# Performance work log

Hardware: AMD Instinct MI355X
Metric: run time of the kernel (lower is better)

The kernel has to match this reference:

```python
import jax, jax.numpy as jnp
import numpy as np

B, K, DIM = 20000, 32, 256
N_ENT, N_USR = 100000, 50000

def _norm_clip(e):
    # torch nn.Embedding(max_norm=1): renormalize looked-up rows to norm <= 1
    n = jnp.linalg.norm(e, axis=-1, keepdims=True)
    return e * jnp.minimum(1.0, 1.0 / jnp.maximum(n, 1e-12))

def setup_inputs() -> dict:
    key = jax.random.key(0)
    ks = jax.random.split(key, 7)
    return {
        "u": jax.random.randint(ks[0], (B,), 0, N_USR),
        "t_idx": jax.random.randint(ks[1], (B,), 0, N_ENT),
        "n_idx": jax.random.randint(ks[2], (B, K), 0, N_ENT),
        "entity_emb": jax.random.normal(ks[3], (N_ENT, DIM), jnp.float32) * 0.1,
        "user_emb": jax.random.normal(ks[4], (N_USR, DIM), jnp.float32) * 0.1,
        "W": jax.random.normal(ks[5], (DIM // 2, DIM), jnp.float32) * 0.05,
        "a": jax.random.normal(ks[6], (DIM,), jnp.float32) * 0.05,
    }

def reference(u, t_idx, n_idx, entity_emb, user_emb, W, a):
    d_half = W.shape[0]
    xt = _norm_clip(entity_emb[t_idx])          # [B, D]
    xn = _norm_clip(entity_emb[n_idx])          # [B, K, D]
    tw = xt @ W.T                               # [B, H]  H = D/2
    nw = jnp.einsum('bkd,hd->bkh', xn, W)       # [B, K, H]
    # a(cat([tw, nw])) = tw @ a[:H] + nw @ a[H:]
    scores = tw @ a[:d_half]                    # [B]
    scores = scores[:, None] + nw @ a[d_half:]  # [B, K]
    e = jnp.where(scores >= 0, scores, 0.2 * scores)  # leaky relu, slope 0.2
    alpha = jax.nn.softmax(e, axis=1)           # softmax over neighbors
    head = jnp.einsum('bk,bkh->bh', alpha, nw)  # [B, H]
    # both "heads" share W and a in the original -> identical outputs, concat
    items = jnp.concatenate([head, head], axis=-1)  # [B, D]
    users = _norm_clip(user_emb[u])             # [B, D]
    uv = jnp.sum(users * items, axis=1)
    return jax.nn.sigmoid(uv)
```

## Files before the change

kernel.cpp:

```cpp
#include <hip/hip_runtime.h>
#include <math.h>

#define B_    20000
#define K_    32
#define DIM_  256
#define H_    128
#define NENT_ 100000

typedef unsigned int   uint_t;
typedef unsigned short ushort_t;
typedef __attribute__((ext_vector_type(8))) short bf16x8;
typedef __attribute__((ext_vector_type(4))) float f32x4;

__device__ __forceinline__ float dot4(float4 a, float4 b) {
    return a.x * b.x + a.y * b.y + a.z * b.z + a.w * b.w;
}

__device__ __forceinline__ float wred64(float v) {
    #pragma unroll
    for (int m = 32; m >= 1; m >>= 1) v += __shfl_xor(v, m, 64);
    return v;
}

__device__ __forceinline__ ushort_t f2bf(float f) {
    uint_t x = __float_as_uint(f);
    uint_t r = (x + 0x7fffu + ((x >> 16) & 1u)) >> 16;
    return (ushort_t)r;
}

__device__ __forceinline__ uint_t pack2(float lo, float hi) {
    return (uint_t)f2bf(lo) | ((uint_t)f2bf(hi) << 16);
}

__launch_bounds__(256)
__global__ void proj_direct(const float* __restrict__ ent,
                            const float* __restrict__ Wm,
                            const float* __restrict__ av,
                            float* __restrict__ sc1,
                            float* __restrict__ sc2,
                            ushort_t* __restrict__ P) {
    __shared__ short Ws[128 * 256];

    const int t    = threadIdx.x;
    const int gb   = blockIdx.x * 128;
    const int lane = t & 63;
    const int w    = t >> 6;
    const int l15  = lane & 15;
    const int l4   = lane >> 4;

    {
        const int r    = t >> 1;
        const int half = (t & 1) * 128;
        const float* wp = Wm + r * DIM_ + half;
        const int swz = (r & 7) << 4;
        #pragma unroll
        for (int jc = 0; jc < 16; ++jc) {
            float4 f0 = *(const float4*)(wp + jc * 8);
            float4 f1 = *(const float4*)(wp + jc * 8 + 4);
            union { bf16x8 v; ushort_t us[8]; } pk;
            pk.us[0] = f2bf(f0.x); pk.us[1] = f2bf(f0.y);
            pk.us[2] = f2bf(f0.z); pk.us[3] = f2bf(f0.w);
            pk.us[4] = f2bf(f1.x); pk.us[5] = f2bf(f1.y);
            pk.us[6] = f2bf(f1.z); pk.us[7] = f2bf(f1.w);
            const int off = (r * 512 + half * 2 + jc * 16) ^ swz;
            *(bf16x8*)((char*)Ws + off) = pk.v;
        }
    }

    const int ebase = gb + w * 32;
    bf16x8 bfr[2][8];
    float scale[2];
    #pragma unroll
    for (int et = 0; et < 2; ++et) {
        const int eg = min(ebase + et * 16 + l15, NENT_ - 1);
        const float* xp = ent + (size_t)eg * DIM_ + l4 * 8;
        float ssq = 0.f;
        #pragma unroll
        for (int kk = 0; kk < 8; ++kk) {
            float4 f0 = *(const float4*)(xp + kk * 32);
            float4 f1 = *(const float4*)(xp + kk * 32 + 4);
            ssq += dot4(f0, f0) + dot4(f1, f1);
            union { bf16x8 v; ushort_t us[8]; } pk;
            pk.us[0] = f2bf(f0.x); pk.us[1] = f2bf(f0.y);
            pk.us[2] = f2bf(f0.z); pk.us[3] = f2bf(f0.w);
            pk.us[4] = f2bf(f1.x); pk.us[5] = f2bf(f1.y);
            pk.us[6] = f2bf(f1.z); pk.us[7] = f2bf(f1.w);
            bfr[et][kk] = pk.v;
        }
        ssq += __shfl_xor(ssq, 16, 64);
        ssq += __shfl_xor(ssq, 32, 64);
        scale[et] = fminf(1.f, 1.f / fmaxf(sqrtf(ssq), 1e-12f));
    }

    __syncthreads();

    float s1[2] = {0.f, 0.f}, s2[2] = {0.f, 0.f};
    #pragma unroll 2
    for (int ht = 0; ht < 8; ++ht) {
        const int hrow = ht * 16 + l15;
        const int hswz = (hrow & 7) << 4;
        bf16x8 af[8];
        #pragma unroll
        for (int kk = 0; kk < 8; ++kk)
            af[kk] = *(const bf16x8*)((const char*)Ws +
                     ((hrow * 512 + kk * 64 + l4 * 16) ^ hswz));
        f32x4 acc0 = (f32x4){0.f, 0.f, 0.f, 0.f};
        f32x4 acc1 = (f32x4){0.f, 0.f, 0.f, 0.f};
        #pragma unroll
        for (int kk = 0; kk < 8; ++kk) {
            acc0 = __builtin_amdgcn_mfma_f32_16x16x32_bf16(af[kk], bfr[0][kk], acc0, 0, 0, 0);
            acc1 = __builtin_amdgcn_mfma_f32_16x16x32_bf16(af[kk], bfr[1][kk], acc1, 0, 0, 0);
        }
        const int hb = ht * 16 + l4 * 4;
        const float4 a1v = *(const float4*)(av + hb);
        const float4 a2v = *(const float4*)(av + H_ + hb);
        #pragma unroll
        for (int et = 0; et < 2; ++et) {
            const f32x4 v = et ? acc1 : acc0;
            const float scl = scale[et];
            const float v0 = v[0] * scl, v1 = v[1] * scl;
            const float v2 = v[2] * scl, v3 = v[3] * scl;
            s1[et] += a1v.x * v0 + a1v.y * v1 + a1v.z * v2 + a1v.w * v3;
            s2[et] += a2v.x * v0 + a2v.y * v1 + a2v.z * v2 + a2v.w * v3;
            const int eg = ebase + et * 16 + l15;
            if (eg < NENT_) {
                uint2 pk;
                pk.x = pack2(v0, v1);
                pk.y = pack2(v2, v3);
                *(uint2*)(P + (size_t)eg * H_ + hb) = pk;
            }
        }
    }

    #pragma unroll
    for (int et = 0; et < 2; ++et) {
        float a1 = s1[et], a2 = s2[et];
        a1 += __shfl_xor(a1, 16, 64);
        a1 += __shfl_xor(a1, 32, 64);
        a2 += __shfl_xor(a2, 16, 64);
        a2 += __shfl_xor(a2, 32, 64);
        const int eg = ebase + et * 16 + l15;
        if (l4 == 0 && eg < NENT_) {
            sc1[eg] = a1;
            sc2[eg] = a2;
        }
    }
}

__launch_bounds__(256)
__global__ void main_kernel(const int* __restrict__ u,
                            const int* __restrict__ t_idx,
                            const int* __restrict__ n_idx,
                            const float* __restrict__ usr,
                            const float* __restrict__ sc1,
                            const float* __restrict__ sc2,
                            const ushort_t* __restrict__ P,
                            float* __restrict__ out) {
    const int wave = threadIdx.x >> 6;
    const int lane = threadIdx.x & 63;
    const int b    = blockIdx.x * 4 + wave;
    const int j    = lane & 31;
    const int q    = lane >> 4;
    const int c    = lane & 15;

    const int nk = n_idx[b * K_ + j];
    int nm[8];
    #pragma unroll
    for (int i = 0; i < 8; ++i) nm[i] = __shfl(nk, i * 4 + q);
    uint4 pv[8];
    #pragma unroll
    for (int i = 0; i < 8; ++i)
        pv[i] = *(const uint4*)((const char*)P + (size_t)nm[i] * 256 + c * 16);

    const float* ubp = usr + (size_t)u[b] * DIM_;
    float4 ua0 = *(const float4*)(ubp + 8 * c);
    float4 ua1 = *(const float4*)(ubp + 8 * c + 4);
    float4 ub0 = *(const float4*)(ubp + H_ + 8 * c);
    float4 ub1 = *(const float4*)(ubp + H_ + 8 * c + 4);

    float s = sc1[t_idx[b]] + sc2[nk];
    s = (s >= 0.f) ? s : 0.2f * s;
    float mx = s;
    #pragma unroll
    for (int m = 16; m >= 1; m >>= 1) mx = fmaxf(mx, __shfl_xor(mx, m, 64));
    float ex = __expf(s - mx);
    float sm = ex;
    #pragma unroll
    for (int m = 16; m >= 1; m >>= 1) sm += __shfl_xor(sm, m, 64);
    const float alpha = ex / sm;

    float ss = dot4(ua0, ua0) + dot4(ua1, ua1) + dot4(ub0, ub0) + dot4(ub1, ub1);
    #pragma unroll
    for (int m = 8; m >= 1; m >>= 1) ss += __shfl_xor(ss, m, 64);
    const float scl = fminf(1.f, 1.f / fmaxf(sqrtf(ss), 1e-12f));
    float uc[8];
    uc[0] = scl * (ua0.x + ub0.x); uc[1] = scl * (ua0.y + ub0.y);
    uc[2] = scl * (ua0.z + ub0.z); uc[3] = scl * (ua0.w + ub0.w);
    uc[4] = scl * (ua1.x + ub1.x); uc[5] = scl * (ua1.y + ub1.y);
    uc[6] = scl * (ua1.z + ub1.z); uc[7] = scl * (ua1.w + ub1.w);

    float sp = 0.f;
    #pragma unroll
    for (int i = 0; i < 8; ++i) {
        const float am = __shfl(alpha, i * 4 + q);
        const uint4 v = pv[i];
        float d;
        d  = uc[0] * __uint_as_float(v.x << 16);
        d += uc[1] * __uint_as_float(v.x & 0xffff0000u);
        d += uc[2] * __uint_as_float(v.y << 16);
        d += uc[3] * __uint_as_float(v.y & 0xffff0000u);
        d += uc[4] * __uint_as_float(v.z << 16);
        d += uc[5] * __uint_as_float(v.z & 0xffff0000u);
        d += uc[6] * __uint_as_float(v.w << 16);
        d += uc[7] * __uint_as_float(v.w & 0xffff0000u);
        sp += am * d;
    }
    sp = wred64(sp);
    if (lane == 0) out[b] = 1.f / (1.f + __expf(-sp));
}

__global__ void precompute_v12(const float* __restrict__ W,
                               const float* __restrict__ a,
                               float* __restrict__ v12) {
    int d = blockIdx.x * blockDim.x + threadIdx.x;
    if (d >= DIM_) return;
    float acc1 = 0.f, acc2 = 0.f;
    for (int h = 0; h < H_; ++h) {
        float w = W[h * DIM_ + d];
        acc1 += a[h] * w;
        acc2 += a[H_ + h] * w;
    }
    v12[d] = acc1;
    v12[DIM_ + d] = acc2;
}

__launch_bounds__(256)
__global__ void gat_main(const int* __restrict__ u,
                         const int* __restrict__ t_idx,
                         const int* __restrict__ n_idx,
                         const float* __restrict__ ent,
                         const float* __restrict__ usr,
                         const float* __restrict__ W,
                         const float* __restrict__ v12,
                         float* __restrict__ out) {
    const int b    = blockIdx.x;
    const int tid  = threadIdx.x;
    const int wave = tid >> 6;
    const int lane = tid & 63;

    __shared__ float xn_s[K_][DIM_];
    __shared__ float scr_s[K_];
    __shared__ float alpha_s[K_];
    __shared__ float uc_s[H_];
    __shared__ float red_s[4];

    const float4 v1_4 = ((const float4*)v12)[lane];
    const float4 v2_4 = ((const float4*)(v12 + DIM_))[lane];

    const int t = t_idx[b];
    float4 t4 = ((const float4*)(ent + (size_t)t * DIM_))[lane];
    float ss_t = wred64(dot4(t4, t4));
    float scl_t = fminf(1.0f, 1.0f / fmaxf(sqrtf(ss_t), 1e-12f));
    float s0 = scl_t * wred64(dot4(t4, v1_4));

    const int uid = u[b];
    float4 u4 = ((const float4*)(usr + (size_t)uid * DIM_))[lane];
    float ss_u = wred64(dot4(u4, u4));
    float scl_u = fminf(1.0f, 1.0f / fmaxf(sqrtf(ss_u), 1e-12f));
    float px = __shfl(u4.x, lane + 32);
    float py = __shfl(u4.y, lane + 32);
    float pz = __shfl(u4.z, lane + 32);
    float pw = __shfl(u4.w, lane + 32);
    if (wave == 0 && lane < 32) {
        float4 uc4;
        uc4.x = scl_u * (u4.x + px);
        uc4.y = scl_u * (u4.y + py);
        uc4.z = scl_u * (u4.z + pz);
        uc4.w = scl_u * (u4.w + pw);
        ((float4*)uc_s)[lane] = uc4;
    }

    for (int kk = 0; kk < 8; ++kk) {
        const int k   = wave * 8 + kk;
        const int idx = n_idx[b * K_ + k];
        float4 e4 = ((const float4*)(ent + (size_t)idx * DIM_))[lane];
        float ssk = wred64(dot4(e4, e4));
        float sk  = fminf(1.0f, 1.0f / fmaxf(sqrtf(ssk), 1e-12f));
        float dv2 = wred64(dot4(e4, v2_4));
        float4 xs;
        xs.x = e4.x * sk; xs.y = e4.y * sk; xs.z = e4.z * sk; xs.w = e4.w * sk;
        ((float4*)xn_s[k])[lane] = xs;
        if (lane == 0) {
            float sc = s0 + sk * dv2;
            scr_s[k] = (sc >= 0.f) ? sc : 0.2f * sc;
        }
    }
    __syncthreads();

    if (tid < 32) {
        float e = scr_s[tid];
        float mx = e;
        #pragma unroll
        for (int m = 16; m >= 1; m >>= 1) mx = fmaxf(mx, __shfl_xor(mx, m, 64));
        float ex = expf(e - mx);
        float sm = ex;
        #pragma unroll
        for (int m = 16; m >= 1; m >>= 1) sm += __shfl_xor(sm, m, 64);
        alpha_s[tid] = ex / sm;
    }
    __syncthreads();

    float m_d = 0.f;
    #pragma unroll
    for (int k = 0; k < K_; ++k) m_d += alpha_s[k] * xn_s[k][tid];

    const float* wcol = W + tid;
    float acc = 0.f;
    #pragma unroll 4
    for (int hh = 0; hh < H_; ++hh) acc += uc_s[hh] * wcol[(size_t)hh * DIM_];

    float p = wred64(acc * m_d);
    if (lane == 0) red_s[wave] = p;
    __syncthreads();
    if (tid == 0) {
        float uv = red_s[0] + red_s[1] + red_s[2] + red_s[3];
        out[b] = 1.0f / (1.0f + expf(-uv));
    }
}

extern "C" void kernel_launch(void* const* d_in, const int* in_sizes, int n_in,
                              void* d_out, int out_size, void* d_ws, size_t ws_size,
                              hipStream_t stream) {
    const int*   u     = (const int*)d_in[0];
    const int*   t_idx = (const int*)d_in[1];
    const int*   n_idx = (const int*)d_in[2];
    const float* ent   = (const float*)d_in[3];
    const float* usr   = (const float*)d_in[4];
    const float* W     = (const float*)d_in[5];
    const float* a     = (const float*)d_in[6];
    float*       out   = (float*)d_out;

    const size_t SC1_OFF = 0;
    const size_t SC2_OFF = (size_t)NENT_ * 4;
    const size_t P_OFF   = (size_t)NENT_ * 8;
    const size_t NEED    = P_OFF + (size_t)NENT_ * H_ * 2;

    if (ws_size >= NEED) {
        float*    sc1 = (float*)((char*)d_ws + SC1_OFF);
        float*    sc2 = (float*)((char*)d_ws + SC2_OFF);
        ushort_t* P   = (ushort_t*)((char*)d_ws + P_OFF);

        hipLaunchKernelGGL(proj_direct, dim3((NENT_ + 127) / 128), dim3(256), 0, stream,
                           ent, W, a, sc1, sc2, P);
        hipLaunchKernelGGL(main_kernel, dim3(B_ / 4), dim3(256), 0, stream,
                           u, t_idx, n_idx, usr, sc1, sc2, P, out);
    } else {
        float* v12 = (float*)d_ws;
        hipLaunchKernelGGL(precompute_v12, dim3(1), dim3(256), 0, stream, W, a, v12);
        hipLaunchKernelGGL(gat_main, dim3(B_), dim3(256), 0, stream,
                           u, t_idx, n_idx, ent, usr, W, v12, out);
    }
}
```

Measured before the change: 237.7 us.

## Pre-convert W to bf16 fragment layout and drop LDS staging in projection

A small prep kernel converts W to bf16 once and stores it in MFMA fragment order in workspace. The projection kernel then reads the A fragments straight from global memory (L2-resident, 64KB) instead of every block converting all of W into a 64KB LDS tile and syncing. Dropping the LDS allocation also allows higher occupancy (launch_bounds 256,4). In exchange it adds an extra launch and repeated global/L2 reads of W per wave, and the workspace requirement grows, which could fall back to the slow path if the workspace is too small.

After: 262.5 us. +10.4%, slower.

```diff
diff --git a/kernel.cpp b/kernel.cpp
--- a/kernel.cpp
+++ b/kernel.cpp
@@ -32,42 +32,38 @@
     return (uint_t)f2bf(lo) | ((uint_t)f2bf(hi) << 16);
 }
 
-__launch_bounds__(256)
-__global__ void proj_direct(const float* __restrict__ ent,
-                            const float* __restrict__ Wm,
-                            const float* __restrict__ av,
-                            float* __restrict__ sc1,
-                            float* __restrict__ sc2,
-                            ushort_t* __restrict__ P) {
-    __shared__ short Ws[128 * 256];
-
+__global__ void w_prep(const float* __restrict__ Wm, ushort_t* __restrict__ Wb) {
+    const int idx  = blockIdx.x * 256 + threadIdx.x;
+    const int lane = idx & 63;
+    const int kk   = (idx >> 6) & 7;
+    const int ht   = idx >> 9;
+    const int h    = ht * 16 + (lane & 15);
+    const int k    = kk * 32 + (lane >> 4) * 8;
+    const float* wp = Wm + h * DIM_ + k;
+    float4 f0 = *(const float4*)(wp);
+    float4 f1 = *(const float4*)(wp + 4);
+    union { bf16x8 v; ushort_t us[8]; } pk;
+    pk.us[0] = f2bf(f0.x); pk.us[1] = f2bf(f0.y);
+    pk.us[2] = f2bf(f0.z); pk.us[3] = f2bf(f0.w);
+    pk.us[4] = f2bf(f1.x); pk.us[5] = f2bf(f1.y);
+    pk.us[6] = f2bf(f1.z); pk.us[7] = f2bf(f1.w);
+    ((bf16x8*)Wb)[idx] = pk.v;
+}
+
+__launch_bounds__(256, 4)
+__global__ void proj_nolds(const float* __restrict__ ent,
+                           const ushort_t* __restrict__ Wb,
+                           const float* __restrict__ av,
+                           float* __restrict__ sc1,
+                           float* __restrict__ sc2,
+                           ushort_t* __restrict__ P) {
     const int t    = threadIdx.x;
-    const int gb   = blockIdx.x * 128;
     const int lane = t & 63;
     const int w    = t >> 6;
     const int l15  = lane & 15;
     const int l4   = lane >> 4;
-
-    {
-        const int r    = t >> 1;
-        const int half = (t & 1) * 128;
-        const float* wp = Wm + r * DIM_ + half;
-        const int swz = (r & 7) << 4;
-        #pragma unroll
-        for (int jc = 0; jc < 16; ++jc) {
-            float4 f0 = *(const float4*)(wp + jc * 8);
-            float4 f1 = *(const float4*)(wp + jc * 8 + 4);
-            union { bf16x8 v; ushort_t us[8]; } pk;
-            pk.us[0] = f2bf(f0.x); pk.us[1] = f2bf(f0.y);
-            pk.us[2] = f2bf(f0.z); pk.us[3] = f2bf(f0.w);
-            pk.us[4] = f2bf(f1.x); pk.us[5] = f2bf(f1.y);
-            pk.us[6] = f2bf(f1.z); pk.us[7] = f2bf(f1.w);
-            const int off = (r * 512 + half * 2 + jc * 16) ^ swz;
-            *(bf16x8*)((char*)Ws + off) = pk.v;
-        }
-    }
-
-    const int ebase = gb + w * 32;
+    const int ebase = blockIdx.x * 128 + w * 32;
+
     bf16x8 bfr[2][8];
     float scale[2];
     #pragma unroll
@@ -92,24 +88,17 @@
         scale[et] = fminf(1.f, 1.f / fmaxf(sqrtf(ssq), 1e-12f));
     }
 
-    __syncthreads();
-
     float s1[2] = {0.f, 0.f}, s2[2] = {0.f, 0.f};
     #pragma unroll 2
     for (int ht = 0; ht < 8; ++ht) {
-        const int hrow = ht * 16 + l15;
-        const int hswz = (hrow & 7) << 4;
-        bf16x8 af[8];
-        #pragma unroll
-        for (int kk = 0; kk < 8; ++kk)
-            af[kk] = *(const bf16x8*)((const char*)Ws +
-                     ((hrow * 512 + kk * 64 + l4 * 16) ^ hswz));
+        const bf16x8* wp = (const bf16x8*)Wb + ht * 512 + lane;
         f32x4 acc0 = (f32x4){0.f, 0.f, 0.f, 0.f};
         f32x4 acc1 = (f32x4){0.f, 0.f, 0.f, 0.f};
         #pragma unroll
         for (int kk = 0; kk < 8; ++kk) {
-            acc0 = __builtin_amdgcn_mfma_f32_16x16x32_bf16(af[kk], bfr[0][kk], acc0, 0, 0, 0);
-            acc1 = __builtin_amdgcn_mfma_f32_16x16x32_bf16(af[kk], bfr[1][kk], acc1, 0, 0, 0);
+            const bf16x8 af = wp[kk * 64];
+            acc0 = __builtin_amdgcn_mfma_f32_16x16x32_bf16(af, bfr[0][kk], acc0, 0, 0, 0);
+            acc1 = __builtin_amdgcn_mfma_f32_16x16x32_bf16(af, bfr[1][kk], acc1, 0, 0, 0);
         }
         const int hb = ht * 16 + l4 * 4;
         const float4 a1v = *(const float4*)(av + hb);
@@ -343,15 +332,18 @@
     const size_t SC1_OFF = 0;
     const size_t SC2_OFF = (size_t)NENT_ * 4;
     const size_t P_OFF   = (size_t)NENT_ * 8;
-    const size_t NEED    = P_OFF + (size_t)NENT_ * H_ * 2;
+    const size_t WB_OFF  = P_OFF + (size_t)NENT_ * H_ * 2;
+    const size_t NEED    = WB_OFF + (size_t)H_ * DIM_ * 2;
 
     if (ws_size >= NEED) {
         float*    sc1 = (float*)((char*)d_ws + SC1_OFF);
         float*    sc2 = (float*)((char*)d_ws + SC2_OFF);
         ushort_t* P   = (ushort_t*)((char*)d_ws + P_OFF);
-
-        hipLaunchKernelGGL(proj_direct, dim3((NENT_ + 127) / 128), dim3(256), 0, stream,
-                           ent, W, a, sc1, sc2, P);
+        ushort_t* Wb  = (ushort_t*)((char*)d_ws + WB_OFF);
+
+        hipLaunchKernelGGL(w_prep, dim3(16), dim3(256), 0, stream, W, Wb);
+        hipLaunchKernelGGL(proj_nolds, dim3((NENT_ + 127) / 128), dim3(256), 0, stream,
+                           ent, Wb, a, sc1, sc2, P);
         hipLaunchKernelGGL(main_kernel, dim3(B_ / 4), dim3(256), 0, stream,
                            u, t_idx, n_idx, usr, sc1, sc2, P, out);
     } else {
```
